# Performance work log

Hardware: AMD Instinct MI355X
Metric: run time of the kernel (lower is better)

## Reference

```python
import jax, jax.numpy as jnp
import numpy as np

PART = 6
FEAT = 1024
DIM_CUT = 8
DC = FEAT // DIM_CUT  # 128
BATCH = 8192
NEG = -1000000.0
LRELU_SLOPE = 0.25
BN_EPS = 1e-5
L2_EPS = 1e-8


def lrelu(x):
    return jnp.where(x >= 0, x, LRELU_SLOPE * x)


def l2norm(x, axis=1):
    n = jnp.sqrt(jnp.sum(x * x, axis=axis, keepdims=True))
    return x / (n + L2_EPS)


def setup_inputs() -> dict:
    key = jax.random.key(0)
    ks = jax.random.split(key, 5)
    x = jax.random.normal(ks[0], (BATCH, FEAT, PART), dtype=jnp.float32)
    w_ps = jax.random.normal(ks[1], (PART, DC, FEAT), dtype=jnp.float32) * 0.02
    w_cs = jax.random.normal(ks[2], (PART, DC, FEAT), dtype=jnp.float32) * 0.02
    w_up = jax.random.normal(ks[3], (PART, FEAT, DC), dtype=jnp.float32) * 0.02
    w_la = jax.random.normal(ks[4], (PART, 512, FEAT), dtype=jnp.float32) * 0.02
    bn_gamma = jnp.ones((PART, FEAT), dtype=jnp.float32)
    bn_beta = jnp.zeros((PART, FEAT), dtype=jnp.float32)
    bn_mean = jnp.zeros((PART, FEAT), dtype=jnp.float32)
    bn_var = jnp.ones((PART, FEAT), dtype=jnp.float32)
    return {"x": x, "w_ps": w_ps, "w_cs": w_cs, "w_up": w_up,
            "bn_gamma": bn_gamma, "bn_beta": bn_beta,
            "bn_mean": bn_mean, "bn_var": bn_var, "w_la": w_la}


def reference(x, w_ps, w_cs, w_up, bn_gamma, bn_beta, bn_mean, bn_var, w_la):
    # x: [B, C=1024, P]. Per-part 1x1 convs == per-part matmuls, batched via einsum.
    ps = lrelu(jnp.einsum('bcp,pkc->bkp', x, w_ps))   # [B, 128, P]
    cs = lrelu(jnp.einsum('bcp,pkc->bkp', x, w_cs))   # [B, 128, P]
    ps_n = l2norm(ps, axis=1)
    cs_n = l2norm(cs, axis=1)
    # masked self-attention over parts
    att = jnp.einsum('bkp,bkq->bpq', ps_n, cs_n)       # [B, P, P]
    att = att + (jnp.eye(PART, dtype=att.dtype) * NEG)[None]
    att = jax.nn.softmax(att, axis=1)                  # torch F.softmax(dim=1)
    emb_att = jnp.einsum('bkp,bpq->bkq', ps_n, att)    # [B, 128, P]
    # per-part up-dim conv + BN(eval) + LReLU
    h = jnp.einsum('bkp,pok->bop', emb_att, w_up)      # [B, 1024, P]
    inv = 1.0 / jnp.sqrt(bn_var + BN_EPS)              # [P, 1024]
    h = (h - bn_mean.T[None]) * (bn_gamma * inv).T[None] + bn_beta.T[None]
    h = lrelu(h)
    emb2 = x + h                                       # residual, [B, 1024, P]
    # per-part local-attention conv (no BN / relu)
    out = jnp.einsum('bcp,poc->bop', emb2, w_la)       # [B, 512, P]
    return out
```

## Files before the change

kernel.cpp:

```cpp
#include <hip/hip_runtime.h>
#include <cstdint>
#include <cstddef>

#define B_N  8192
#define FEAT 1024
#define PART 6
#define DC   128
#define OUTC 512

typedef __bf16 bf16;
typedef bf16 bf16x8 __attribute__((ext_vector_type(8)));
typedef bf16 bf16x2 __attribute__((ext_vector_type(2)));
typedef float f32x4 __attribute__((ext_vector_type(4)));

__device__ __forceinline__ void gload16(const bf16* g, bf16* l) {
  __builtin_amdgcn_global_load_lds(
      (const __attribute__((address_space(1))) void*)g,
      (__attribute__((address_space(3))) void*)l, 16, 0, 0);
}

__global__ void k_f2b(const float* __restrict__ s, bf16* __restrict__ d, int n) {
  int i = blockIdx.x * 256 + threadIdx.x;
  if (i < n) d[i] = (bf16)s[i];
}

__global__ void k_bn(const float* __restrict__ g, const float* __restrict__ be,
                     const float* __restrict__ m, const float* __restrict__ v,
                     float* __restrict__ sc, float* __restrict__ sh) {
  int i = blockIdx.x * 256 + threadIdx.x;
  if (i < PART * FEAT) {
    float inv = 1.0f / sqrtf(v[i] + 1e-5f);
    float s = g[i] * inv;
    sc[i] = s;
    sh[i] = be[i] - m[i] * s;
  }
}

__global__ void k_transpose_x(const float* __restrict__ x, bf16* __restrict__ xT) {
  int t = blockIdx.x * 256 + threadIdx.x;
  int b = t >> 9;
  int c0 = (t & 511) << 1;
  const float4* src = (const float4*)(x + ((size_t)b * FEAT + c0) * PART);
  float4 v0 = src[0], v1 = src[1], v2 = src[2];
  float e[12] = {v0.x, v0.y, v0.z, v0.w, v1.x, v1.y, v1.z, v1.w, v2.x, v2.y, v2.z, v2.w};
#pragma unroll
  for (int p = 0; p < PART; ++p) {
    bf16x2 w; w.x = (bf16)e[p]; w.y = (bf16)e[6 + p];
    *(bf16x2*)(xT + ((size_t)p * B_N + b) * FEAT + c0) = w;
  }
}

template <int EPI, int K, int N>
__global__ __launch_bounds__(256) void k_gemm(
    const bf16* __restrict__ Abase, const bf16* __restrict__ Wbase,
    float* __restrict__ Fout, bf16* __restrict__ Bout,
    const float* __restrict__ bnsc, const float* __restrict__ bnsh,
    const bf16* __restrict__ resid) {
  __shared__ bf16 As[128 * 64];
  __shared__ bf16 Ws[128 * 64];
  const int tid = threadIdx.x;
  const int wv = tid >> 6, lane = tid & 63;
  const int wr = wv >> 1, wc = wv & 1;
  const int l = lane & 15, hh = lane >> 4;
  const int tm = blockIdx.x, tn = blockIdx.y, z = blockIdx.z;

  int ap = (EPI == 0) ? (z < PART ? z : z - PART) : z;
  const bf16* A = Abase + (size_t)ap * B_N * K + (size_t)tm * 128 * K;
  const bf16* W = Wbase + (size_t)z * N * K + (size_t)tn * 128 * K;

  f32x4 acc[4][4] = {};

  for (int kt = 0; kt < K / 64; ++kt) {
    __syncthreads();
#pragma unroll
    for (int it = 0; it < 4; ++it) {
      int s = it * 256 + wv * 64 + lane;
      int r = s >> 3;
      int c = (s & 7) ^ (r & 7);
      gload16(A + (size_t)r * K + kt * 64 + c * 8, &As[(it * 256 + wv * 64) * 8]);
      gload16(W + (size_t)r * K + kt * 64 + c * 8, &Ws[(it * 256 + wv * 64) * 8]);
    }
    asm volatile("s_waitcnt vmcnt(0)" ::: "memory");
    __syncthreads();
#pragma unroll
    for (int kk = 0; kk < 2; ++kk) {
      bf16x8 af[4], wf[4];
#pragma unroll
      for (int mi = 0; mi < 4; ++mi) {
        int row = wr * 64 + mi * 16 + l;
        int c = (kk * 4 + hh) ^ (row & 7);
        af[mi] = *(const bf16x8*)&As[row * 64 + c * 8];
      }
#pragma unroll
      for (int ni = 0; ni < 4; ++ni) {
        int row = wc * 64 + ni * 16 + l;
        int c = (kk * 4 + hh) ^ (row & 7);
        wf[ni] = *(const bf16x8*)&Ws[row * 64 + c * 8];
      }
#pragma unroll
      for (int mi = 0; mi < 4; ++mi)
#pragma unroll
        for (int ni = 0; ni < 4; ++ni)
          acc[mi][ni] = __builtin_amdgcn_mfma_f32_16x16x32_bf16(af[mi], wf[ni], acc[mi][ni], 0, 0, 0);
    }
  }

#pragma unroll
  for (int mi = 0; mi < 4; ++mi)
#pragma unroll
    for (int ni = 0; ni < 4; ++ni)
#pragma unroll
      for (int r = 0; r < 4; ++r) {
        int row = tm * 128 + wr * 64 + mi * 16 + hh * 4 + r;
        int col = tn * 128 + wc * 64 + ni * 16 + l;
        float v = acc[mi][ni][r];
        if constexpr (EPI == 0) {
          v = v >= 0.f ? v : 0.25f * v;
          Fout[(size_t)z * B_N * N + (size_t)row * N + col] = v;
        } else if constexpr (EPI == 1) {
          v = v * bnsc[z * N + col] + bnsh[z * N + col];
          v = v >= 0.f ? v : 0.25f * v;
          v += (float)resid[((size_t)z * B_N + row) * N + col];
          Bout[((size_t)z * B_N + row) * N + col] = (bf16)v;
        } else {
          Fout[((size_t)z * B_N + row) * N + col] = v;
        }
      }
}

__global__ __launch_bounds__(256) void k_att(const float* __restrict__ ps,
                                             const float* __restrict__ cs,
                                             bf16* __restrict__ embT) {
  int wv = threadIdx.x >> 6, lane = threadIdx.x & 63;
  int b = blockIdx.x * 4 + wv;
  float p0[6], p1[6], c0[6], c1[6];
#pragma unroll
  for (int p = 0; p < 6; ++p) {
    float2 v = *(const float2*)(ps + ((size_t)p * B_N + b) * DC + 2 * lane);
    p0[p] = v.x; p1[p] = v.y;
    float2 u = *(const float2*)(cs + ((size_t)p * B_N + b) * DC + 2 * lane);
    c0[p] = u.x; c1[p] = u.y;
  }
  float red[48];
#pragma unroll
  for (int p = 0; p < 6; ++p) {
    red[p] = p0[p] * p0[p] + p1[p] * p1[p];
    red[6 + p] = c0[p] * c0[p] + c1[p] * c1[p];
  }
#pragma unroll
  for (int p = 0; p < 6; ++p)
#pragma unroll
    for (int q = 0; q < 6; ++q)
      red[12 + p * 6 + q] = p0[p] * c0[q] + p1[p] * c1[q];
#pragma unroll
  for (int m = 1; m < 64; m <<= 1)
#pragma unroll
    for (int i = 0; i < 48; ++i)
      red[i] += __shfl_xor(red[i], m, 64);

  float inp[6], inc[6];
#pragma unroll
  for (int p = 0; p < 6; ++p) {
    inp[p] = 1.f / (sqrtf(red[p]) + 1e-8f);
    inc[p] = 1.f / (sqrtf(red[6 + p]) + 1e-8f);
  }
  float att[6][6];
#pragma unroll
  for (int p = 0; p < 6; ++p)
#pragma unroll
    for (int q = 0; q < 6; ++q)
      att[p][q] = red[12 + p * 6 + q] * inp[p] * inc[q] + (p == q ? -1000000.f : 0.f);
#pragma unroll
  for (int q = 0; q < 6; ++q) {
    float mx = att[0][q];
#pragma unroll
    for (int p = 1; p < 6; ++p) mx = fmaxf(mx, att[p][q]);
    float e[6], s = 0.f;
#pragma unroll
    for (int p = 0; p < 6; ++p) { e[p] = expf(att[p][q] - mx); s += e[p]; }
    float is = 1.f / s;
#pragma unroll
    for (int p = 0; p < 6; ++p) att[p][q] = e[p] * is;
  }
#pragma unroll
  for (int q = 0; q < 6; ++q) {
    float e0 = 0.f, e1 = 0.f;
#pragma unroll
    for (int p = 0; p < 6; ++p) {
      float a = att[p][q] * inp[p];
      e0 += p0[p] * a; e1 += p1[p] * a;
    }
    bf16x2 w; w.x = (bf16)e0; w.y = (bf16)e1;
    *(bf16x2*)(embT + ((size_t)q * B_N + b) * DC + 2 * lane) = w;
  }
}

__global__ void k_transpose_out(const float* __restrict__ oT, float* __restrict__ out) {
  int t = blockIdx.x * 256 + threadIdx.x;
  int b = t >> 8;
  int o0 = (t & 255) << 1;
  float a[6], c[6];
#pragma unroll
  for (int p = 0; p < 6; ++p) {
    float2 v = *(const float2*)(oT + ((size_t)p * B_N + b) * OUTC + o0);
    a[p] = v.x; c[p] = v.y;
  }
  float* dst = out + ((size_t)b * OUTC + o0) * PART;
  float4 w0 = {a[0], a[1], a[2], a[3]};
  float4 w1 = {a[4], a[5], c[0], c[1]};
  float4 w2 = {c[2], c[3], c[4], c[5]};
  ((float4*)dst)[0] = w0; ((float4*)dst)[1] = w1; ((float4*)dst)[2] = w2;
}

extern "C" void kernel_launch(void* const* d_in, const int* in_sizes, int n_in,
                              void* d_out, int out_size, void* d_ws, size_t ws_size,
                              hipStream_t stream) {
  const float* x    = (const float*)d_in[0];
  const float* w_ps = (const float*)d_in[1];
  const float* w_cs = (const float*)d_in[2];
  const float* w_up = (const float*)d_in[3];
  const float* gam  = (const float*)d_in[4];
  const float* bet  = (const float*)d_in[5];
  const float* mea  = (const float*)d_in[6];
  const float* var  = (const float*)d_in[7];
  const float* w_la = (const float*)d_in[8];

  char* ws = (char*)d_ws;
  size_t off = 0;
  auto alloc = [&](size_t bytes) { void* p = ws + off; off += (bytes + 255) & ~(size_t)255; return p; };

  bf16* xT    = (bf16*)alloc((size_t)PART * B_N * FEAT * 2);
  bf16* wpsb  = (bf16*)alloc((size_t)2 * PART * DC * FEAT * 2);
  bf16* wupb  = (bf16*)alloc((size_t)PART * FEAT * DC * 2);
  bf16* wlab  = (bf16*)alloc((size_t)PART * OUTC * FEAT * 2);
  float* bnsc = (float*)alloc((size_t)PART * FEAT * 4);
  float* bnsh = (float*)alloc((size_t)PART * FEAT * 4);
  float* psb  = (float*)alloc((size_t)2 * PART * B_N * DC * 4);
  bf16* embT  = (bf16*)alloc((size_t)PART * B_N * DC * 2);
  bf16* emb2T = (bf16*)alloc((size_t)PART * B_N * FEAT * 2);
  float* outT = (float*)xT;

  const int nw = PART * DC * FEAT;
  const int nl = PART * OUTC * FEAT;
  k_f2b<<<(nw + 255) / 256, 256, 0, stream>>>(w_ps, wpsb, nw);
  k_f2b<<<(nw + 255) / 256, 256, 0, stream>>>(w_cs, wpsb + nw, nw);
  k_f2b<<<(nw + 255) / 256, 256, 0, stream>>>(w_up, wupb, nw);
  k_f2b<<<(nl + 255) / 256, 256, 0, stream>>>(w_la, wlab, nl);
  k_bn<<<(PART * FEAT + 255) / 256, 256, 0, stream>>>(gam, bet, mea, var, bnsc, bnsh);
  k_transpose_x<<<B_N * 512 / 256, 256, 0, stream>>>(x, xT);

  k_gemm<0, FEAT, DC><<<dim3(64, 1, 12), 256, 0, stream>>>(
      xT, wpsb, psb, nullptr, nullptr, nullptr, nullptr);
  k_att<<<B_N / 4, 256, 0, stream>>>(psb, psb + (size_t)PART * B_N * DC, embT);
  k_gemm<1, DC, FEAT><<<dim3(64, 8, 6), 256, 0, stream>>>(
      embT, wupb, nullptr, emb2T, bnsc, bnsh, xT);
  k_gemm<2, FEAT, OUTC><<<dim3(64, 4, 6), 256, 0, stream>>>(
      emb2T, wlab, outT, nullptr, nullptr, nullptr, nullptr);
  k_transpose_out<<<B_N * 256 / 256, 256, 0, stream>>>(outT, (float*)d_out);
}
```

Baseline: 666.6 us.

## Merge prep kernels, store intermediates in bf16, interleave ps/cs weights, remap workgroups

Folds the four weight-conversion launches and the BN-fold launch into a single prep kernel. The ps and cs weights are interleaved per part, so the first GEMM covers N=256 on one A panel rather than two separate z-slices. The ps/cs activations and the final GEMM output are now written as bf16 instead of fp32, roughly halving intermediate traffic at some precision cost. A 1D grid with an XCD-aware block remap (bid&7 strided) is meant to keep tiles that share A/W panels on the same XCD for L2 reuse.

```diff
diff --git a/kernel.cpp b/kernel.cpp
--- a/kernel.cpp
+++ b/kernel.cpp
@@ -19,20 +19,28 @@
       (__attribute__((address_space(3))) void*)l, 16, 0, 0);
 }
 
-__global__ void k_f2b(const float* __restrict__ s, bf16* __restrict__ d, int n) {
+__global__ void k_prep(const float* __restrict__ w_ps, const float* __restrict__ w_cs,
+                       const float* __restrict__ w_up, const float* __restrict__ w_la,
+                       const float* __restrict__ g, const float* __restrict__ be,
+                       const float* __restrict__ m, const float* __restrict__ v,
+                       bf16* __restrict__ wpsb, bf16* __restrict__ wupb,
+                       bf16* __restrict__ wlab, float* __restrict__ bnsc,
+                       float* __restrict__ bnsh) {
   int i = blockIdx.x * 256 + threadIdx.x;
-  if (i < n) d[i] = (bf16)s[i];
-}
-
-__global__ void k_bn(const float* __restrict__ g, const float* __restrict__ be,
-                     const float* __restrict__ m, const float* __restrict__ v,
-                     float* __restrict__ sc, float* __restrict__ sh) {
-  int i = blockIdx.x * 256 + threadIdx.x;
+  const int NW = PART * DC * FEAT;
+  const int NL = PART * OUTC * FEAT;
+  if (i < NW) {
+    int z = i / (DC * FEAT), r = i % (DC * FEAT);
+    wpsb[(size_t)(2 * z) * DC * FEAT + r] = (bf16)w_ps[i];
+    wpsb[(size_t)(2 * z + 1) * DC * FEAT + r] = (bf16)w_cs[i];
+    wupb[i] = (bf16)w_up[i];
+  }
+  if (i < NL) wlab[i] = (bf16)w_la[i];
   if (i < PART * FEAT) {
     float inv = 1.0f / sqrtf(v[i] + 1e-5f);
     float s = g[i] * inv;
-    sc[i] = s;
-    sh[i] = be[i] - m[i] * s;
+    bnsc[i] = s;
+    bnsh[i] = be[i] - m[i] * s;
   }
 }
 
@@ -50,10 +58,10 @@
   }
 }
 
-template <int EPI, int K, int N>
+template <int EPI, int K, int N, int TM, int TN, int NZ>
 __global__ __launch_bounds__(256) void k_gemm(
     const bf16* __restrict__ Abase, const bf16* __restrict__ Wbase,
-    float* __restrict__ Fout, bf16* __restrict__ Bout,
+    bf16* __restrict__ Out,
     const float* __restrict__ bnsc, const float* __restrict__ bnsh,
     const bf16* __restrict__ resid) {
   __shared__ bf16 As[128 * 64];
@@ -62,10 +70,16 @@
   const int wv = tid >> 6, lane = tid & 63;
   const int wr = wv >> 1, wc = wv & 1;
   const int l = lane & 15, hh = lane >> 4;
-  const int tm = blockIdx.x, tn = blockIdx.y, z = blockIdx.z;
-
-  int ap = (EPI == 0) ? (z < PART ? z : z - PART) : z;
-  const bf16* A = Abase + (size_t)ap * B_N * K + (size_t)tm * 128 * K;
+
+  constexpr int NWG = TM * TN * NZ;
+  constexpr int QC = NWG / 8;
+  int bid = blockIdx.x;
+  int lid = (bid & 7) * QC + (bid >> 3);
+  int tn = lid % TN;
+  int tm = (lid / TN) % TM;
+  int z = lid / (TN * TM);
+
+  const bf16* A = Abase + (size_t)z * B_N * K + (size_t)tm * 128 * K;
   const bf16* W = Wbase + (size_t)z * N * K + (size_t)tn * 128 * K;
 
   f32x4 acc[4][4] = {};
@@ -116,30 +130,27 @@
         float v = acc[mi][ni][r];
         if constexpr (EPI == 0) {
           v = v >= 0.f ? v : 0.25f * v;
-          Fout[(size_t)z * B_N * N + (size_t)row * N + col] = v;
         } else if constexpr (EPI == 1) {
           v = v * bnsc[z * N + col] + bnsh[z * N + col];
           v = v >= 0.f ? v : 0.25f * v;
           v += (float)resid[((size_t)z * B_N + row) * N + col];
-          Bout[((size_t)z * B_N + row) * N + col] = (bf16)v;
-        } else {
-          Fout[((size_t)z * B_N + row) * N + col] = v;
         }
+        Out[((size_t)z * B_N + row) * N + col] = (bf16)v;
       }
 }
 
-__global__ __launch_bounds__(256) void k_att(const float* __restrict__ ps,
-                                             const float* __restrict__ cs,
+__global__ __launch_bounds__(256) void k_att(const bf16* __restrict__ psb,
                                              bf16* __restrict__ embT) {
   int wv = threadIdx.x >> 6, lane = threadIdx.x & 63;
   int b = blockIdx.x * 4 + wv;
   float p0[6], p1[6], c0[6], c1[6];
 #pragma unroll
   for (int p = 0; p < 6; ++p) {
-    float2 v = *(const float2*)(ps + ((size_t)p * B_N + b) * DC + 2 * lane);
-    p0[p] = v.x; p1[p] = v.y;
-    float2 u = *(const float2*)(cs + ((size_t)p * B_N + b) * DC + 2 * lane);
-    c0[p] = u.x; c1[p] = u.y;
+    const bf16* base = psb + ((size_t)p * B_N + b) * 256;
+    bf16x2 v = *(const bf16x2*)(base + 2 * lane);
+    p0[p] = (float)v.x; p1[p] = (float)v.y;
+    bf16x2 u = *(const bf16x2*)(base + 128 + 2 * lane);
+    c0[p] = (float)u.x; c1[p] = (float)u.y;
   }
   float red[48];
 #pragma unroll
@@ -195,15 +206,15 @@
   }
 }
 
-__global__ void k_transpose_out(const float* __restrict__ oT, float* __restrict__ out) {
+__global__ void k_transpose_out(const bf16* __restrict__ oT, float* __restrict__ out) {
   int t = blockIdx.x * 256 + threadIdx.x;
   int b = t >> 8;
   int o0 = (t & 255) << 1;
   float a[6], c[6];
 #pragma unroll
   for (int p = 0; p < 6; ++p) {
-    float2 v = *(const float2*)(oT + ((size_t)p * B_N + b) * OUTC + o0);
-    a[p] = v.x; c[p] = v.y;
+    bf16x2 v = *(const bf16x2*)(oT + ((size_t)p * B_N + b) * OUTC + o0);
+    a[p] = (float)v.x; c[p] = (float)v.y;
   }
   float* dst = out + ((size_t)b * OUTC + o0) * PART;
   float4 w0 = {a[0], a[1], a[2], a[3]};
@@ -230,31 +241,26 @@
   auto alloc = [&](size_t bytes) { void* p = ws + off; off += (bytes + 255) & ~(size_t)255; return p; };
 
   bf16* xT    = (bf16*)alloc((size_t)PART * B_N * FEAT * 2);
-  bf16* wpsb  = (bf16*)alloc((size_t)2 * PART * DC * FEAT * 2);
+  bf16* wpsb  = (bf16*)alloc((size_t)PART * 256 * FEAT * 2);
   bf16* wupb  = (bf16*)alloc((size_t)PART * FEAT * DC * 2);
   bf16* wlab  = (bf16*)alloc((size_t)PART * OUTC * FEAT * 2);
   float* bnsc = (float*)alloc((size_t)PART * FEAT * 4);
   float* bnsh = (float*)alloc((size_t)PART * FEAT * 4);
-  float* psb  = (float*)alloc((size_t)2 * PART * B_N * DC * 4);
+  bf16* psb   = (bf16*)alloc((size_t)PART * B_N * 256 * 2);
   bf16* embT  = (bf16*)alloc((size_t)PART * B_N * DC * 2);
   bf16* emb2T = (bf16*)alloc((size_t)PART * B_N * FEAT * 2);
-  float* outT = (float*)xT;
-
-  const int nw = PART * DC * FEAT;
-  const int nl = PART * OUTC * FEAT;
-  k_f2b<<<(nw + 255) / 256, 256, 0, stream>>>(w_ps, wpsb, nw);
-  k_f2b<<<(nw + 255) / 256, 256, 0, stream>>>(w_cs, wpsb + nw, nw);
-  k_f2b<<<(nw + 255) / 256, 256, 0, stream>>>(w_up, wupb, nw);
-  k_f2b<<<(nl + 255) / 256, 256, 0, stream>>>(w_la, wlab, nl);
-  k_bn<<<(PART * FEAT + 255) / 256, 256, 0, stream>>>(gam, bet, mea, var, bnsc, bnsh);
+  bf16* outT  = xT;
+
+  k_prep<<<(PART * OUTC * FEAT + 255) / 256, 256, 0, stream>>>(
+      w_ps, w_cs, w_up, w_la, gam, bet, mea, var, wpsb, wupb, wlab, bnsc, bnsh);
   k_transpose_x<<<B_N * 512 / 256, 256, 0, stream>>>(x, xT);
 
-  k_gemm<0, FEAT, DC><<<dim3(64, 1, 12), 256, 0, stream>>>(
-      xT, wpsb, psb, nullptr, nullptr, nullptr, nullptr);
-  k_att<<<B_N / 4, 256, 0, stream>>>(psb, psb + (size_t)PART * B_N * DC, embT);
-  k_gemm<1, DC, FEAT><<<dim3(64, 8, 6), 256, 0, stream>>>(
-      embT, wupb, nullptr, emb2T, bnsc, bnsh, xT);
-  k_gemm<2, FEAT, OUTC><<<dim3(64, 4, 6), 256, 0, stream>>>(
-      emb2T, wlab, outT, nullptr, nullptr, nullptr, nullptr);
+  k_gemm<0, FEAT, 256, 64, 2, 6><<<768, 256, 0, stream>>>(
+      xT, wpsb, psb, nullptr, nullptr, nullptr);
+  k_att<<<B_N / 4, 256, 0, stream>>>(psb, embT);
+  k_gemm<1, DC, FEAT, 64, 8, 6><<<3072, 256, 0, stream>>>(
+      embT, wupb, emb2T, bnsc, bnsh, xT);
+  k_gemm<2, FEAT, OUTC, 64, 4, 6><<<1536, 256, 0, stream>>>(
+      emb2T, wlab, outT, nullptr, nullptr, nullptr);
   k_transpose_out<<<B_N * 256 / 256, 256, 0, stream>>>(outT, (float*)d_out);
 }
```

Measured after the change: 615.9 us. 7.6% less time.
